# Performance work log

Hardware: AMD Instinct MI355X
Metric: run time of the kernel (lower is better)

## Reference

```python
import jax, jax.numpy as jnp
import numpy as np

EPS = 1e-5

def conv(x, w, b=None, groups=1):
    kh, kw = w.shape[2], w.shape[3]
    y = jax.lax.conv_general_dilated(
        x, w, (1, 1), ((kh // 2, kh // 2), (kw // 2, kw // 2)),
        dimension_numbers=('NCHW', 'OIHW', 'NCHW'), feature_group_count=groups)
    if b is not None:
        y = y + b[None, :, None, None]
    return y

def layernorm_c(x, g, b):
    # LayerNorm over channel dim (module permutes to NHWC, norms last dim, permutes back)
    mu = jnp.mean(x, axis=1, keepdims=True)
    var = jnp.mean(jnp.square(x - mu), axis=1, keepdims=True)
    return (x - mu) * jax.lax.rsqrt(var + EPS) * g[None, :, None, None] + b[None, :, None, None]

def _bilinear(img, py, px):
    # img: (N,C,H,W); py,px: (N,H,W) float sampling coords; zero outside bounds
    H, W = img.shape[2], img.shape[3]
    y0 = jnp.floor(py); x0 = jnp.floor(px)
    wy1 = py - y0; wy0 = 1.0 - wy1
    wx1 = px - x0; wx0 = 1.0 - wx1

    def gather(yc, xc):
        valid = (yc >= 0) & (yc <= H - 1) & (xc >= 0) & (xc <= W - 1)
        yi = jnp.clip(yc, 0, H - 1).astype(jnp.int32)
        xi = jnp.clip(xc, 0, W - 1).astype(jnp.int32)
        v = jax.vmap(lambda im, yy, xx: im[:, yy, xx])(img, yi, xi)  # (N,C,H,W)
        return v * valid[:, None].astype(img.dtype)

    return (gather(y0, x0) * (wy0 * wx0)[:, None]
            + gather(y0, x0 + 1) * (wy0 * wx1)[:, None]
            + gather(y0 + 1, x0) * (wy1 * wx0)[:, None]
            + gather(y0 + 1, x0 + 1) * (wy1 * wx1)[:, None])

def deform_conv2d(x, offset, weight, mask):
    # torchvision-style modulated deformable conv, 3x3, pad=1, stride=1
    N, C, H, W = x.shape
    by, bx = jnp.meshgrid(jnp.arange(H, dtype=x.dtype), jnp.arange(W, dtype=x.dtype), indexing='ij')
    out = jnp.zeros((N, weight.shape[0], H, W), dtype=x.dtype)
    for i in range(3):
        for j in range(3):
            k = i * 3 + j
            py = by[None] + (i - 1) + offset[:, 2 * k]      # (N,H,W)
            px = bx[None] + (j - 1) + offset[:, 2 * k + 1]
            samp = _bilinear(x, py, px) * mask[:, k][:, None]  # (N,C,H,W)
            out = out + jnp.einsum('nchw,oc->nohw', samp, weight[:, :, i, j])
    return out

def _forward(input_flow, input_event,
             ln_flow_g, ln_flow_b, ln_event_g, ln_event_b,
             ff_w1, ff_b1, ff_w2, ff_b2,
             fo_w1, fo_b1, fo_w2, fo_b2,
             fm_w1, fm_b1, fm_w2, fm_b2,
             dc_weight,
             sf_w1, sf_b1, sf_w2, sf_b2, sf_w3, sf_b3, sf_w4, sf_b4,
             fl_w1, fl_b1, fl_w2, fl_b2):
    N, C, H, W = input_flow.shape
    flow_norm = layernorm_c(input_flow, ln_flow_g, ln_flow_b)
    event_norm = layernorm_c(input_event, ln_event_g, ln_event_b)
    x = conv(jax.nn.relu(conv(flow_norm, ff_w1, ff_b1)), ff_w2, ff_b2, groups=C)
    offset = conv(jax.nn.relu(conv(event_norm, fo_w1, fo_b1)), fo_w2, fo_b2)
    mask = jax.nn.sigmoid(conv(jax.nn.relu(conv(event_norm, fm_w1, fm_b1)), fm_w2, fm_b2))
    dc = deform_conv2d(x, offset, dc_weight, mask)
    x_fft = jnp.fft.rfft2(x)            # (N,C,H,W//2+1) complex
    dc_fft = jnp.fft.rfft2(dc)
    fft_cate = jnp.concatenate([dc_fft.real, dc_fft.imag], axis=1)  # (N,2C,H,Wf)
    h = conv(fft_cate, sf_w1, sf_b1)
    h = conv(h, sf_w2, sf_b2, groups=2 * C)
    h = jax.nn.relu(conv(h, sf_w3, sf_b3))
    sp_mask = jax.nn.sigmoid(conv(h, sf_w4, sf_b4))  # (N,C,H,Wf) real
    x_irfft = jnp.fft.irfft2(x_fft * sp_mask, s=(H, W))
    g = conv(x_irfft, fl_w1, fl_b1, groups=C)
    a, b = jnp.split(g, 2, axis=1)
    g = a * jax.nn.gelu(b, approximate=False)
    return conv(g, fl_w2, fl_b2) + input_flow

def setup_inputs() -> dict:
    key = jax.random.key(0)
    N, C, H, W = 8, 32, 256, 256
    ks = iter(jax.random.split(key, 64))
    rn = lambda shp, s=0.05: jax.random.normal(next(ks), shp, dtype=jnp.float32) * s
    d = {
        'input_flow': jax.random.normal(next(ks), (N, C, H, W), dtype=jnp.float32),
        'input_event': jax.random.normal(next(ks), (N, C, H, W), dtype=jnp.float32),
        'ln_flow_g': 1.0 + rn((C,), 0.1), 'ln_flow_b': rn((C,), 0.1),
        'ln_event_g': 1.0 + rn((C,), 0.1), 'ln_event_b': rn((C,), 0.1),
        'ff_w1': rn((C, C, 1, 1)), 'ff_b1': rn((C,)),
        'ff_w2': rn((C, 1, 3, 3)), 'ff_b2': rn((C,)),
        'fo_w1': rn((C, C, 1, 1)), 'fo_b1': rn((C,)),
        'fo_w2': rn((18, C, 3, 3)), 'fo_b2': rn((18,)),
        'fm_w1': rn((C, C, 1, 1)), 'fm_b1': rn((C,)),
        'fm_w2': rn((9, C, 3, 3)), 'fm_b2': rn((9,)),
        'dc_weight': rn((C, C, 3, 3)),
        'sf_w1': rn((2 * C, 2 * C, 1, 1)), 'sf_b1': rn((2 * C,)),
        'sf_w2': rn((2 * C, 1, 3, 3)), 'sf_b2': rn((2 * C,)),
        'sf_w3': rn((2 * C, 2 * C, 1, 1)), 'sf_b3': rn((2 * C,)),
        'sf_w4': rn((C, 2 * C, 1, 1)), 'sf_b4': rn((C,)),
        'fl_w1': rn((C, 1, 3, 3)), 'fl_b1': rn((C,)),
        'fl_w2': rn((C, C // 2, 1, 1)), 'fl_b2': rn((C,)),
    }
    return d

def reference(input_flow, input_event,
              ln_flow_g, ln_flow_b, ln_event_g, ln_event_b,
              ff_w1, ff_b1, ff_w2, ff_b2,
              fo_w1, fo_b1, fo_w2, fo_b2,
              fm_w1, fm_b1, fm_w2, fm_b2,
              dc_weight,
              sf_w1, sf_b1, sf_w2, sf_b2, sf_w3, sf_b3, sf_w4, sf_b4,
              fl_w1, fl_b1, fl_w2, fl_b2):
    return _forward(input_flow, input_event,
                    ln_flow_g, ln_flow_b, ln_event_g, ln_event_b,
                    ff_w1, ff_b1, ff_w2, ff_b2,
                    fo_w1, fo_b1, fo_w2, fo_b2,
                    fm_w1, fm_b1, fm_w2, fm_b2,
                    dc_weight,
                    sf_w1, sf_b1, sf_w2, sf_b2, sf_w3, sf_b3, sf_w4, sf_b4,
                    fl_w1, fl_b1, fl_w2, fl_b2)
```

## Files before the change

kernel.cpp:

```cpp
#include <hip/hip_runtime.h>
#include <cmath>

constexpr int kN = 8;
constexpr int kC = 32;
constexpr int kH = 256;
constexpr int kW = 256;
constexpr int kHW = kH * kW;
constexpr int kWF = 129;
constexpr int kHWF = kH * kWF;
constexpr float kPI = 3.14159265358979323846f;

__device__ __forceinline__ float sigmoidf_(float x) { return 1.f / (1.f + expf(-x)); }

__device__ __forceinline__ int xcd_swizzle(int bid, int nblk)
{
    int chunk = nblk >> 3;
    return (bid & 7) * chunk + (bid >> 3);
}

template <bool TWO>
__global__ __launch_bounds__(256) void lnmv_kernel(
    const float* __restrict__ in,
    const float* __restrict__ lng, const float* __restrict__ lnb,
    const float* __restrict__ w1, const float* __restrict__ b1, float* __restrict__ out1,
    const float* __restrict__ w2, const float* __restrict__ b2, float* __restrict__ out2)
{
    __shared__ __align__(16) float wl1[1024];
    __shared__ __align__(16) float wl2[TWO ? 1024 : 4];
    __shared__ float bl1[32], bl2[32], gl[32], bbl[32];
    int tid = threadIdx.x;
    for (int e = tid; e < 1024; e += 256) {
        wl1[e] = w1[e];
        if (TWO) wl2[e] = w2[e];
    }
    if (tid < 32) {
        bl1[tid] = b1[tid]; gl[tid] = lng[tid]; bbl[tid] = lnb[tid];
        if (TWO) bl2[tid] = b2[tid];
    }
    __syncthreads();

    int p = blockIdx.x * 256 + tid;
    int n = p >> 16;
    int rem = p & 65535;
    const float* base = in + (size_t)n * kC * kHW + rem;

    float v[32];
    float mu = 0.f;
#pragma unroll
    for (int c = 0; c < 32; ++c) { v[c] = base[(size_t)c * kHW]; mu += v[c]; }
    mu *= 0.03125f;
    float var = 0.f;
#pragma unroll
    for (int c = 0; c < 32; ++c) { float d = v[c] - mu; var += d * d; }
    var *= 0.03125f;
    float rs = rsqrtf(var + 1e-5f);
#pragma unroll
    for (int c = 0; c < 32; ++c) v[c] = (v[c] - mu) * rs * gl[c] + bbl[c];

    {
        float* o = out1 + (size_t)n * kC * kHW + rem;
#pragma unroll
        for (int oc = 0; oc < 32; ++oc) {
            const float4* wr = reinterpret_cast<const float4*>(wl1 + oc * 32);
            float acc = bl1[oc];
#pragma unroll
            for (int q = 0; q < 8; ++q) {
                float4 wv = wr[q];
                acc += wv.x * v[4*q] + wv.y * v[4*q+1] + wv.z * v[4*q+2] + wv.w * v[4*q+3];
            }
            o[(size_t)oc * kHW] = fmaxf(acc, 0.f);
        }
    }
    if (TWO) {
        float* o = out2 + (size_t)n * kC * kHW + rem;
#pragma unroll
        for (int oc = 0; oc < 32; ++oc) {
            const float4* wr = reinterpret_cast<const float4*>(wl2 + oc * 32);
            float acc = bl2[oc];
#pragma unroll
            for (int q = 0; q < 8; ++q) {
                float4 wv = wr[q];
                acc += wv.x * v[4*q] + wv.y * v[4*q+1] + wv.z * v[4*q+2] + wv.w * v[4*q+3];
            }
            o[(size_t)oc * kHW] = fmaxf(acc, 0.f);
        }
    }
}

__global__ __launch_bounds__(256) void dw3x3_kernel(
    const float* __restrict__ in, const float* __restrict__ w,
    const float* __restrict__ bias, float* __restrict__ out,
    int CH, int Hd, int Wd, int total)
{
    int sw = xcd_swizzle(blockIdx.x, gridDim.x);
    int idx = sw * 256 + threadIdx.x;
    if (idx >= total) return;
    int wx = idx % Wd;
    int rest = idx / Wd;
    int hy = rest % Hd;
    int pl = rest / Hd;
    int ch = pl % CH;

    const float* ip = in + (size_t)pl * Hd * Wd;
    const float* wp = w + ch * 9;
    float acc = bias[ch];
#pragma unroll
    for (int dy = -1; dy <= 1; ++dy) {
        int yy = hy + dy;
        if (yy < 0 || yy >= Hd) continue;
        const float* rp = ip + (size_t)yy * Wd;
#pragma unroll
        for (int dx = -1; dx <= 1; ++dx) {
            int xx = wx + dx;
            if (xx < 0 || xx >= Wd) continue;
            acc += rp[xx] * wp[(dy + 1) * 3 + (dx + 1)];
        }
    }
    out[idx] = acc;
}

template <int COUT, int COUTP, int ACT>
__global__ __launch_bounds__(256) void conv3x3_kernel(
    const float* __restrict__ in, const float* __restrict__ wg,
    const float* __restrict__ bias, float* __restrict__ out)
{
    __shared__ __align__(16) float wl[288 * COUTP];
    __shared__ float bl[COUT];
    int tid = threadIdx.x;
    for (int e = tid; e < 288 * COUTP; e += 256) {
        int oc = e % COUTP;
        int t = e / COUTP;
        wl[e] = (oc < COUT) ? wg[(oc * 32 + (t / 9)) * 9 + (t % 9)] : 0.f;
    }
    if (tid < COUT) bl[tid] = bias[tid];
    __syncthreads();

    int sw = xcd_swizzle(blockIdx.x, gridDim.x);
    int row = sw * 4 + (tid >> 6);
    int lane = tid & 63;
    int n = row >> 8;
    int h = row & 255;

    float acc[4][COUTP];
#pragma unroll
    for (int px = 0; px < 4; ++px)
#pragma unroll
        for (int oc = 0; oc < COUTP; ++oc) acc[px][oc] = (oc < COUT) ? bl[oc] : 0.f;

    const float* ib = in + (size_t)n * 32 * kHW;
    for (int ic = 0; ic < 32; ++ic) {
        const float* ipl = ib + (size_t)ic * kHW;
#pragma unroll
        for (int ky = 0; ky < 3; ++ky) {
            int yy = h + ky - 1;
            if (yy < 0 || yy > 255) continue;
            const float* rp = ipl + (size_t)yy * 256;
#pragma unroll
            for (int kx = 0; kx < 3; ++kx) {
                float val[4];
#pragma unroll
                for (int px = 0; px < 4; ++px) {
                    int xx = lane + px * 64 + kx - 1;
                    val[px] = (xx >= 0 && xx < 256) ? rp[xx] : 0.f;
                }
                const float4* wr = reinterpret_cast<const float4*>(wl + (ic * 9 + ky * 3 + kx) * COUTP);
#pragma unroll
                for (int q = 0; q < COUTP / 4; ++q) {
                    float4 wv = wr[q];
#pragma unroll
                    for (int px = 0; px < 4; ++px) {
                        acc[px][4*q+0] += val[px] * wv.x;
                        acc[px][4*q+1] += val[px] * wv.y;
                        acc[px][4*q+2] += val[px] * wv.z;
                        acc[px][4*q+3] += val[px] * wv.w;
                    }
                }
            }
        }
    }

    float* ob = out + (size_t)n * COUT * kHW + (size_t)h * 256;
#pragma unroll
    for (int oc = 0; oc < COUT; ++oc) {
#pragma unroll
        for (int px = 0; px < 4; ++px) {
            float r = acc[px][oc];
            if (ACT == 2) r = sigmoidf_(r);
            ob[(size_t)oc * kHW + lane + px * 64] = r;
        }
    }
}

__global__ __launch_bounds__(256) void deform_kernel(
    const float* __restrict__ x, const float* __restrict__ off,
    const float* __restrict__ msk, const float* __restrict__ wt,
    float* __restrict__ out)
{
    __shared__ __align__(16) float wl[9 * 32 * 32];
    int tid = threadIdx.x;
    for (int e = tid; e < 9216; e += 256) {
        int o = e & 31;
        int t = e >> 5;
        int c = t & 31;
        int k = t >> 5;
        wl[e] = wt[((size_t)(o * 32 + c)) * 9 + k];
    }
    __syncthreads();

    int sw = xcd_swizzle(blockIdx.x, gridDim.x);
    int halfid = tid >> 7;
    int l = tid & 127;
    int row = sw * 2 + halfid;
    int n = row >> 8;
    int h = row & 255;
    int pixbase = h * 256 + l;

    const float* offb = off + (size_t)n * 18 * kHW + pixbase;
    const float* mskb = msk + (size_t)n * 9 * kHW + pixbase;
    const float* xb = x + (size_t)n * 32 * kHW;

    float acc[2][32];
#pragma unroll
    for (int px = 0; px < 2; ++px)
#pragma unroll
        for (int oc = 0; oc < 32; ++oc) acc[px][oc] = 0.f;

    for (int k = 0; k < 9; ++k) {
        int ki = k / 3 - 1, kj = k % 3 - 1;
        int i00[2], i01[2], i10[2], i11[2];
        float w00[2], w01[2], w10[2], w11[2];
#pragma unroll
        for (int px = 0; px < 2; ++px) {
            int wx = l + px * 128;
            float oy = offb[(size_t)(2 * k) * kHW + px * 128];
            float ox = offb[(size_t)(2 * k + 1) * kHW + px * 128];
            float m = mskb[(size_t)k * kHW + px * 128];
            float py = (float)(h + ki) + oy;
            float pxx = (float)(wx + kj) + ox;
            float y0f = floorf(py), x0f = floorf(pxx);
            float fy = py - y0f, fx = pxx - x0f;
            float vy0 = (y0f >= 0.f && y0f <= 255.f) ? 1.f : 0.f;
            float vy1 = (y0f >= -1.f && y0f <= 254.f) ? 1.f : 0.f;
            float vx0 = (x0f >= 0.f && x0f <= 255.f) ? 1.f : 0.f;
            float vx1 = (x0f >= -1.f && x0f <= 254.f) ? 1.f : 0.f;
            int y0 = min(max((int)y0f, 0), 255);
            int y1 = min(max((int)y0f + 1, 0), 255);
            int x0 = min(max((int)x0f, 0), 255);
            int x1 = min(max((int)x0f + 1, 0), 255);
            i00[px] = y0 * 256 + x0; i01[px] = y0 * 256 + x1;
            i10[px] = y1 * 256 + x0; i11[px] = y1 * 256 + x1;
            w00[px] = (1.f - fy) * (1.f - fx) * m * vy0 * vx0;
            w01[px] = (1.f - fy) * fx * m * vy0 * vx1;
            w10[px] = fy * (1.f - fx) * m * vy1 * vx0;
            w11[px] = fy * fx * m * vy1 * vx1;
        }
#pragma unroll 2
        for (int c = 0; c < 32; ++c) {
            const float* xp = xb + (size_t)c * kHW;
            float s[2];
#pragma unroll
            for (int px = 0; px < 2; ++px) {
                s[px] = w00[px] * xp[i00[px]] + w01[px] * xp[i01[px]] +
                        w10[px] * xp[i10[px]] + w11[px] * xp[i11[px]];
            }
            const float4* wr = reinterpret_cast<const float4*>(wl + (size_t)(k * 32 + c) * 32);
#pragma unroll
            for (int q = 0; q < 8; ++q) {
                float4 wv = wr[q];
#pragma unroll
                for (int px = 0; px < 2; ++px) {
                    acc[px][4*q+0] += s[px] * wv.x;
                    acc[px][4*q+1] += s[px] * wv.y;
                    acc[px][4*q+2] += s[px] * wv.z;
                    acc[px][4*q+3] += s[px] * wv.w;
                }
            }
        }
    }

    float* ob = out + (size_t)n * 32 * kHW + pixbase;
#pragma unroll
    for (int oc = 0; oc < 32; ++oc)
#pragma unroll
        for (int px = 0; px < 2; ++px)
            ob[(size_t)oc * kHW + px * 128] = acc[px][oc];
}

__device__ __forceinline__ void fft256_stages(float2* A, float2* Bb, const float2* tw,
                                              int lane, float sgn)
{
    float2* src = A;
    float2* dst = Bb;
#pragma unroll
    for (int s = 0; s < 4; ++s) {
        int m = 1 << (2 * s);
        int r = lane & (m - 1);
        int mc = lane - r;
        __syncthreads();
        float2 x0 = src[lane];
        float2 x1 = src[lane + 128];
        float2 x2 = src[lane + 64];
        float2 x3 = src[lane + 192];
        float2 wa = tw[mc];
        float2 wb = tw[mc + 64];
        float2 wc = tw[2 * mc];
        float way = wa.y * sgn, wby = wb.y * sgn, wcy = wc.y * sgn;
        float e1x = x0.x + x1.x, e1y = x0.y + x1.y;
        float d1x = x0.x - x1.x, d1y = x0.y - x1.y;
        float o1x = wa.x * d1x - way * d1y, o1y = wa.x * d1y + way * d1x;
        float e2x = x2.x + x3.x, e2y = x2.y + x3.y;
        float d2x = x2.x - x3.x, d2y = x2.y - x3.y;
        float o2x = wb.x * d2x - wby * d2y, o2y = wb.x * d2y + wby * d2x;
        int base = r + 4 * mc;
        float2 y0; y0.x = e1x + e2x; y0.y = e1y + e2y;
        float ex = e1x - e2x, ey = e1y - e2y;
        float2 y2; y2.x = wc.x * ex - wcy * ey; y2.y = wc.x * ey + wcy * ex;
        float2 y1; y1.x = o1x + o2x; y1.y = o1y + o2y;
        float ox = o1x - o2x, oy = o1y - o2y;
        float2 y3; y3.x = wc.x * ox - wcy * oy; y3.y = wc.x * oy + wcy * ox;
        dst[base] = y0;
        dst[base + m] = y1;
        dst[base + 2 * m] = y2;
        dst[base + 3 * m] = y3;
        float2* t = src; src = dst; dst = t;
    }
    __syncthreads();
}

__device__ __forceinline__ void fft256_stages16(float2* A, float2* Bb, const float2* tw,
                                                int t, int c, float sgn)
{
    float2* src = A;
    float2* dst = Bb;
#pragma unroll
    for (int s = 0; s < 4; ++s) {
        int m = 1 << (2 * s);
        __syncthreads();
#pragma unroll
        for (int b = 0; b < 4; ++b) {
            int q = t + (b << 4);
            int r = q & (m - 1);
            int mc = q - r;
            float2 x0 = src[q * 17 + c];
            float2 x1 = src[(q + 128) * 17 + c];
            float2 x2 = src[(q + 64) * 17 + c];
            float2 x3 = src[(q + 192) * 17 + c];
            float2 wa = tw[mc];
            float2 wb = tw[mc + 64];
            float2 wc = tw[2 * mc];
            float way = wa.y * sgn, wby = wb.y * sgn, wcy = wc.y * sgn;
            float e1x = x0.x + x1.x, e1y = x0.y + x1.y;
            float d1x = x0.x - x1.x, d1y = x0.y - x1.y;
            float o1x = wa.x * d1x - way * d1y, o1y = wa.x * d1y + way * d1x;
            float e2x = x2.x + x3.x, e2y = x2.y + x3.y;
            float d2x = x2.x - x3.x, d2y = x2.y - x3.y;
            float o2x = wb.x * d2x - wby * d2y, o2y = wb.x * d2y + wby * d2x;
            int base = r + 4 * mc;
            float2 y0; y0.x = e1x + e2x; y0.y = e1y + e2y;
            float ex = e1x - e2x, ey = e1y - e2y;
            float2 y2; y2.x = wc.x * ex - wcy * ey; y2.y = wc.x * ey + wcy * ex;
            float2 y1; y1.x = o1x + o2x; y1.y = o1y + o2y;
            float ox = o1x - o2x, oy = o1y - o2y;
            float2 y3; y3.x = wc.x * ox - wcy * oy; y3.y = wc.x * oy + wcy * ox;
            dst[base * 17 + c] = y0;
            dst[(base + m) * 17 + c] = y1;
            dst[(base + 2 * m) * 17 + c] = y2;
            dst[(base + 3 * m) * 17 + c] = y3;
        }
        float2* tp = src; src = dst; dst = tp;
    }
    __syncthreads();
}

__device__ __forceinline__ void make_tw(float2* tw, int tid)
{
    if (tid < 128) {
        float ang = -kPI * (float)tid / 128.f;
        float2 w; w.x = cosf(ang); w.y = sinf(ang);
        tw[tid] = w;
    }
}

__global__ __launch_bounds__(256) void fft_rows_r2c(const float* __restrict__ in,
                                                    float2* __restrict__ out)
{
    __shared__ float2 A[4][256];
    __shared__ float2 Bb[4][256];
    __shared__ float2 tw[128];
    int tid = threadIdx.x;
    int sub = tid >> 6, lane = tid & 63;
    make_tw(tw, tid);
    size_t row = (size_t)blockIdx.x * 4 + sub;
    const float* rp = in + row * 256;
#pragma unroll
    for (int r = 0; r < 4; ++r) {
        int i = lane + 64 * r;
        float2 a; a.x = rp[i]; a.y = 0.f;
        A[sub][i] = a;
    }
    fft256_stages(A[sub], Bb[sub], tw, lane, 1.f);
    float2* op = out + row * kWF;
    op[lane] = A[sub][lane];
    op[lane + 64] = A[sub][lane + 64];
    if (lane == 0) op[128] = A[sub][128];
}

__global__ __launch_bounds__(256) void fft_cols16(float2* __restrict__ buf)
{
    __shared__ float2 A[256 * 17];
    __shared__ float2 Bb[256 * 17];
    __shared__ float2 tw[128];
    int tid = threadIdx.x;
    make_tw(tw, tid);
    int b = xcd_swizzle(blockIdx.x, gridDim.x);
    int p = b / 9;
    int grp = b % 9;
    int col0 = grp * 16;
    int ncols = (col0 + 16 <= kWF) ? 16 : (kWF - col0);
    float2* base = buf + (size_t)p * kHWF + col0;
    for (int e = tid; e < 4096; e += 256) {
        int pp = e >> 4, cc = e & 15;
        if (cc < ncols) A[pp * 17 + cc] = base[(size_t)pp * kWF + cc];
    }
    int c = tid & 15, t = tid >> 4;
    fft256_stages16(A, Bb, tw, t, c, 1.f);
    for (int e = tid; e < 4096; e += 256) {
        int pp = e >> 4, cc = e & 15;
        if (cc < ncols) base[(size_t)pp * kWF + cc] = A[pp * 17 + cc];
    }
}

__global__ __launch_bounds__(256) void ifft_cols_mask16(const float2* __restrict__ xf,
                                                        const float* __restrict__ spm,
                                                        float2* __restrict__ out)
{
    __shared__ float2 A[256 * 17];
    __shared__ float2 Bb[256 * 17];
    __shared__ float2 tw[128];
    int tid = threadIdx.x;
    make_tw(tw, tid);
    int b = xcd_swizzle(blockIdx.x, gridDim.x);
    int p = b / 9;
    int grp = b % 9;
    int col0 = grp * 16;
    int ncols = (col0 + 16 <= kWF) ? 16 : (kWF - col0);
    const float2* xb = xf + (size_t)p * kHWF + col0;
    const float* mb = spm + (size_t)p * kHWF + col0;
    for (int e = tid; e < 4096; e += 256) {
        int pp = e >> 4, cc = e & 15;
        if (cc < ncols) {
            float2 a = xb[(size_t)pp * kWF + cc];
            float m = mb[(size_t)pp * kWF + cc];
            a.x *= m; a.y *= m;
            A[pp * 17 + cc] = a;
        }
    }
    int c = tid & 15, t = tid >> 4;
    fft256_stages16(A, Bb, tw, t, c, -1.f);
    float2* ob = out + (size_t)p * kHWF + col0;
    for (int e = tid; e < 4096; e += 256) {
        int pp = e >> 4, cc = e & 15;
        if (cc < ncols) ob[(size_t)pp * kWF + cc] = A[pp * 17 + cc];
    }
}

__global__ __launch_bounds__(256) void ifft_rows_c2r(const float2* __restrict__ in,
                                                     float* __restrict__ out)
{
    __shared__ float2 A[4][256];
    __shared__ float2 Bb[4][256];
    __shared__ float2 tw[128];
    int tid = threadIdx.x;
    int sub = tid >> 6, lane = tid & 63;
    make_tw(tw, tid);
    size_t row = (size_t)blockIdx.x * 4 + sub;
    const float2* ip = in + row * kWF;
#pragma unroll
    for (int r = 0; r < 4; ++r) {
        int k = lane + 64 * r;
        if (k <= 128) {
            A[sub][k] = ip[k];
        } else {
            float2 c = ip[256 - k];
            c.y = -c.y;
            A[sub][k] = c;
        }
    }
    fft256_stages(A[sub], Bb[sub], tw, lane, -1.f);
    float* op = out + row * 256;
#pragma unroll
    for (int r = 0; r < 4; ++r) {
        int k = lane + 64 * r;
        op[k] = A[sub][k].x * (1.f / 65536.f);
    }
}

template <int CIN, int COUT, int ACT, bool CPLX>
__global__ __launch_bounds__(256) void conv1x1_kernel(
    const void* __restrict__ inv, const float* __restrict__ wg,
    const float* __restrict__ bias, float* __restrict__ out)
{
    constexpr int PL = kHWF;
    __shared__ __align__(16) float wl[COUT * CIN];
    __shared__ float bl[COUT];
    int tid = threadIdx.x;
    for (int e = tid; e < COUT * CIN; e += 256) wl[e] = wg[e];
    if (tid < COUT) bl[tid] = bias[tid];
    __syncthreads();

    int p0 = blockIdx.x * 256 + tid;
    int n0 = p0 / PL, r0 = p0 % PL;

    float v0[CIN];
    if (CPLX) {
        const float2* in2 = (const float2*)inv;
#pragma unroll
        for (int c = 0; c < 32; ++c) {
            float2 a = in2[(size_t)(n0 * 32 + c) * PL + r0];
            v0[c] = a.x; v0[32 + c] = a.y;
        }
    } else {
        const float* inf_ = (const float*)inv;
#pragma unroll
        for (int c = 0; c < CIN; ++c) {
            v0[c] = inf_[(size_t)(n0 * CIN + c) * PL + r0];
        }
    }

#pragma unroll
    for (int oc = 0; oc < COUT; ++oc) {
        const float4* wr = reinterpret_cast<const float4*>(wl + oc * CIN);
        float a0 = bl[oc];
#pragma unroll
        for (int q = 0; q < CIN / 4; ++q) {
            float4 wv = wr[q];
            a0 += wv.x * v0[4*q] + wv.y * v0[4*q+1] + wv.z * v0[4*q+2] + wv.w * v0[4*q+3];
        }
        if (ACT == 1) a0 = fmaxf(a0, 0.f);
        if (ACT == 2) a0 = sigmoidf_(a0);
        out[(size_t)(n0 * COUT + oc) * PL + r0] = a0;
    }
}

__global__ __launch_bounds__(256) void conv1x1_chain_kernel(
    const float* __restrict__ in, const float* __restrict__ w3,
    const float* __restrict__ b3, const float* __restrict__ w4,
    const float* __restrict__ b4, float* __restrict__ out)
{
    constexpr int PL = kHWF;
    __shared__ __align__(16) float wl3[64 * 64];
    __shared__ __align__(16) float wl4[32 * 64];
    __shared__ float bl3[64], bl4[32];
    int tid = threadIdx.x;
    for (int e = tid; e < 4096; e += 256) wl3[e] = w3[e];
    for (int e = tid; e < 2048; e += 256) wl4[e] = w4[e];
    if (tid < 64) bl3[tid] = b3[tid];
    if (tid < 32) bl4[tid] = b4[tid];
    __syncthreads();

    int p0 = blockIdx.x * 256 + tid;
    int n0 = p0 / PL, r0 = p0 % PL;

    float v0[64];
#pragma unroll
    for (int c = 0; c < 64; ++c) v0[c] = in[(size_t)(n0 * 64 + c) * PL + r0];

    float t0[64];
#pragma unroll
    for (int oc = 0; oc < 64; ++oc) {
        const float4* wr = reinterpret_cast<const float4*>(wl3 + oc * 64);
        float a0 = bl3[oc];
#pragma unroll
        for (int q = 0; q < 16; ++q) {
            float4 wv = wr[q];
            a0 += wv.x * v0[4*q] + wv.y * v0[4*q+1] + wv.z * v0[4*q+2] + wv.w * v0[4*q+3];
        }
        t0[oc] = fmaxf(a0, 0.f);
    }

#pragma unroll
    for (int oc = 0; oc < 32; ++oc) {
        const float4* wr = reinterpret_cast<const float4*>(wl4 + oc * 64);
        float a0 = bl4[oc];
#pragma unroll
        for (int q = 0; q < 16; ++q) {
            float4 wv = wr[q];
            a0 += wv.x * t0[4*q] + wv.y * t0[4*q+1] + wv.z * t0[4*q+2] + wv.w * t0[4*q+3];
        }
        out[(size_t)(n0 * 32 + oc) * PL + r0] = sigmoidf_(a0);
    }
}

__global__ __launch_bounds__(256) void final_kernel(
    const float* __restrict__ g, const float* __restrict__ flow,
    const float* __restrict__ wg, const float* __restrict__ bias,
    float* __restrict__ out)
{
    __shared__ __align__(16) float wl[32 * 16];
    __shared__ float bl[32];
    int tid = threadIdx.x;
    for (int e = tid; e < 512; e += 256) wl[e] = wg[e];
    if (tid < 32) bl[tid] = bias[tid];
    __syncthreads();

    int p = blockIdx.x * 256 + tid;
    int n = p >> 16;
    int rem = p & 65535;
    const float* gb = g + (size_t)n * 32 * kHW + rem;

    float v[16];
#pragma unroll
    for (int c = 0; c < 16; ++c) {
        float a = gb[(size_t)c * kHW];
        float b = gb[(size_t)(16 + c) * kHW];
        float ge = 0.5f * b * (1.f + erff(b * 0.70710678118654752f));
        v[c] = a * ge;
    }

    const float* fb = flow + (size_t)n * 32 * kHW + rem;
    float* ob = out + (size_t)n * 32 * kHW + rem;
#pragma unroll
    for (int oc = 0; oc < 32; ++oc) {
        const float4* wr = reinterpret_cast<const float4*>(wl + oc * 16);
        float acc = bl[oc];
#pragma unroll
        for (int q = 0; q < 4; ++q) {
            float4 wv = wr[q];
            acc += wv.x * v[4*q] + wv.y * v[4*q+1] + wv.z * v[4*q+2] + wv.w * v[4*q+3];
        }
        ob[(size_t)oc * kHW] = acc + fb[(size_t)oc * kHW];
    }
}

extern "C" void kernel_launch(void* const* d_in, const int* in_sizes, int n_in,
                              void* d_out, int out_size, void* d_ws, size_t ws_size,
                              hipStream_t stream)
{
    (void)in_sizes; (void)n_in; (void)out_size; (void)ws_size;

    const float* input_flow  = (const float*)d_in[0];
    const float* input_event = (const float*)d_in[1];
    const float* ln_flow_g   = (const float*)d_in[2];
    const float* ln_flow_b   = (const float*)d_in[3];
    const float* ln_event_g  = (const float*)d_in[4];
    const float* ln_event_b  = (const float*)d_in[5];
    const float* ff_w1 = (const float*)d_in[6];
    const float* ff_b1 = (const float*)d_in[7];
    const float* ff_w2 = (const float*)d_in[8];
    const float* ff_b2 = (const float*)d_in[9];
    const float* fo_w1 = (const float*)d_in[10];
    const float* fo_b1 = (const float*)d_in[11];
    const float* fo_w2 = (const float*)d_in[12];
    const float* fo_b2 = (const float*)d_in[13];
    const float* fm_w1 = (const float*)d_in[14];
    const float* fm_b1 = (const float*)d_in[15];
    const float* fm_w2 = (const float*)d_in[16];
    const float* fm_b2 = (const float*)d_in[17];
    const float* dc_weight = (const float*)d_in[18];
    const float* sf_w1 = (const float*)d_in[19];
    const float* sf_b1 = (const float*)d_in[20];
    const float* sf_w2 = (const float*)d_in[21];
    const float* sf_b2 = (const float*)d_in[22];
    const float* sf_w3 = (const float*)d_in[23];
    const float* sf_b3 = (const float*)d_in[24];
    const float* sf_w4 = (const float*)d_in[25];
    const float* sf_b4 = (const float*)d_in[26];
    const float* fl_w1 = (const float*)d_in[27];
    const float* fl_b1 = (const float*)d_in[28];
    const float* fl_w2 = (const float*)d_in[29];
    const float* fl_b2 = (const float*)d_in[30];
    float* out = (float*)d_out;

    const size_t S = (size_t)16908288;
    float* A = (float*)d_ws;
    float* B = A + S;
    float* Cs = B + S;
    float* X = out;

    lnmv_kernel<false><<<2048, 256, 0, stream>>>(input_flow, ln_flow_g, ln_flow_b,
                                                 ff_w1, ff_b1, A,
                                                 nullptr, nullptr, nullptr);
    lnmv_kernel<true><<<2048, 256, 0, stream>>>(input_event, ln_event_g, ln_event_b,
                                                fo_w1, fo_b1, B,
                                                fm_w1, fm_b1, Cs);
    dw3x3_kernel<<<65536, 256, 0, stream>>>(A, ff_w2, ff_b2, X, 32, 256, 256, 16777216);
    conv3x3_kernel<18, 20, 0><<<512, 256, 0, stream>>>(B, fo_w2, fo_b2, A);
    conv3x3_kernel<9, 12, 2><<<512, 256, 0, stream>>>(Cs, fm_w2, fm_b2, B);
    deform_kernel<<<1024, 256, 0, stream>>>(X, A, B, dc_weight, Cs);
    fft_rows_r2c<<<16384, 256, 0, stream>>>(X, (float2*)A);
    fft_cols16<<<2304, 256, 0, stream>>>((float2*)A);
    fft_rows_r2c<<<16384, 256, 0, stream>>>(Cs, (float2*)B);
    fft_cols16<<<2304, 256, 0, stream>>>((float2*)B);
    conv1x1_kernel<64, 64, 0, true><<<1032, 256, 0, stream>>>((const void*)B, sf_w1, sf_b1, Cs);
    dw3x3_kernel<<<66048, 256, 0, stream>>>(Cs, sf_w2, sf_b2, B, 64, 256, 129, 16908288);
    conv1x1_chain_kernel<<<1032, 256, 0, stream>>>(B, sf_w3, sf_b3, sf_w4, sf_b4, Cs);
    ifft_cols_mask16<<<2304, 256, 0, stream>>>((const float2*)A, Cs, (float2*)B);
    ifft_rows_c2r<<<16384, 256, 0, stream>>>((const float2*)B, Cs);
    dw3x3_kernel<<<65536, 256, 0, stream>>>(Cs, fl_w1, fl_b1, A, 32, 256, 256, 16777216);
    final_kernel<<<2048, 256, 0, stream>>>(A, input_flow, fl_w2, fl_b2, out);
}
```

Before: 1.447 ms.

## Split output channels across blocks in offset conv and deformable conv kernels

The 18-output-channel offset conv now splits its output channels into two halves of 9 handled by separate blocks, doubling the grid. The deformable conv kernel is restructured so each block covers 16 output channels and 4 rows at 4 pixels per thread, instead of 32 channels over 2 rows. The goal is more blocks and lower per-thread register pressure, which should raise occupancy. The cost is redundant input loads and bilinear gathers, since every sample is now computed twice, once per channel half.

```diff
diff --git a/kernel.cpp b/kernel.cpp
--- a/kernel.cpp
+++ b/kernel.cpp
@@ -119,24 +119,26 @@
     out[idx] = acc;
 }
 
-template <int COUT, int COUTP, int ACT>
+template <int COUTTOT, int COUTH, int COUTP, int ACT, int NSPL>
 __global__ __launch_bounds__(256) void conv3x3_kernel(
     const float* __restrict__ in, const float* __restrict__ wg,
     const float* __restrict__ bias, float* __restrict__ out)
 {
     __shared__ __align__(16) float wl[288 * COUTP];
-    __shared__ float bl[COUT];
-    int tid = threadIdx.x;
+    __shared__ float bl[COUTH];
+    int tid = threadIdx.x;
+    int sw = xcd_swizzle(blockIdx.x, gridDim.x);
+    int rowblk = sw / NSPL;
+    int ocbase = (sw % NSPL) * COUTH;
     for (int e = tid; e < 288 * COUTP; e += 256) {
         int oc = e % COUTP;
         int t = e / COUTP;
-        wl[e] = (oc < COUT) ? wg[(oc * 32 + (t / 9)) * 9 + (t % 9)] : 0.f;
-    }
-    if (tid < COUT) bl[tid] = bias[tid];
+        wl[e] = (oc < COUTH) ? wg[((ocbase + oc) * 32 + (t / 9)) * 9 + (t % 9)] : 0.f;
+    }
+    if (tid < COUTH) bl[tid] = bias[ocbase + tid];
     __syncthreads();
 
-    int sw = xcd_swizzle(blockIdx.x, gridDim.x);
-    int row = sw * 4 + (tid >> 6);
+    int row = rowblk * 4 + (tid >> 6);
     int lane = tid & 63;
     int n = row >> 8;
     int h = row & 255;
@@ -145,7 +147,7 @@
 #pragma unroll
     for (int px = 0; px < 4; ++px)
 #pragma unroll
-        for (int oc = 0; oc < COUTP; ++oc) acc[px][oc] = (oc < COUT) ? bl[oc] : 0.f;
+        for (int oc = 0; oc < COUTP; ++oc) acc[px][oc] = (oc < COUTH) ? bl[oc] : 0.f;
 
     const float* ib = in + (size_t)n * 32 * kHW;
     for (int ic = 0; ic < 32; ++ic) {
@@ -179,9 +181,9 @@
         }
     }
 
-    float* ob = out + (size_t)n * COUT * kHW + (size_t)h * 256;
-#pragma unroll
-    for (int oc = 0; oc < COUT; ++oc) {
+    float* ob = out + (size_t)n * COUTTOT * kHW + (size_t)ocbase * kHW + (size_t)h * 256;
+#pragma unroll
+    for (int oc = 0; oc < COUTH; ++oc) {
 #pragma unroll
         for (int px = 0; px < 4; ++px) {
             float r = acc[px][oc];
@@ -196,45 +198,46 @@
     const float* __restrict__ msk, const float* __restrict__ wt,
     float* __restrict__ out)
 {
-    __shared__ __align__(16) float wl[9 * 32 * 32];
-    int tid = threadIdx.x;
-    for (int e = tid; e < 9216; e += 256) {
-        int o = e & 31;
-        int t = e >> 5;
+    __shared__ __align__(16) float wl[9 * 32 * 16];
+    int tid = threadIdx.x;
+    int sw = xcd_swizzle(blockIdx.x, gridDim.x);
+    int rowblk = sw >> 1;
+    int ocbase = (sw & 1) * 16;
+    for (int e = tid; e < 4608; e += 256) {
+        int o = e & 15;
+        int t = e >> 4;
         int c = t & 31;
         int k = t >> 5;
-        wl[e] = wt[((size_t)(o * 32 + c)) * 9 + k];
+        wl[e] = wt[((size_t)((ocbase + o) * 32 + c)) * 9 + k];
     }
     __syncthreads();
 
-    int sw = xcd_swizzle(blockIdx.x, gridDim.x);
-    int halfid = tid >> 7;
-    int l = tid & 127;
-    int row = sw * 2 + halfid;
+    int row = rowblk * 4 + (tid >> 6);
+    int lane = tid & 63;
     int n = row >> 8;
     int h = row & 255;
-    int pixbase = h * 256 + l;
+    int pixbase = h * 256 + lane;
 
     const float* offb = off + (size_t)n * 18 * kHW + pixbase;
     const float* mskb = msk + (size_t)n * 9 * kHW + pixbase;
     const float* xb = x + (size_t)n * 32 * kHW;
 
-    float acc[2][32];
-#pragma unroll
-    for (int px = 0; px < 2; ++px)
-#pragma unroll
-        for (int oc = 0; oc < 32; ++oc) acc[px][oc] = 0.f;
+    float acc[4][16];
+#pragma unroll
+    for (int px = 0; px < 4; ++px)
+#pragma unroll
+        for (int oc = 0; oc < 16; ++oc) acc[px][oc] = 0.f;
 
     for (int k = 0; k < 9; ++k) {
         int ki = k / 3 - 1, kj = k % 3 - 1;
-        int i00[2], i01[2], i10[2], i11[2];
-        float w00[2], w01[2], w10[2], w11[2];
-#pragma unroll
-        for (int px = 0; px < 2; ++px) {
-            int wx = l + px * 128;
-            float oy = offb[(size_t)(2 * k) * kHW + px * 128];
-            float ox = offb[(size_t)(2 * k + 1) * kHW + px * 128];
-            float m = mskb[(size_t)k * kHW + px * 128];
+        int i00[4], i01[4], i10[4], i11[4];
+        float w00[4], w01[4], w10[4], w11[4];
+#pragma unroll
+        for (int px = 0; px < 4; ++px) {
+            int wx = lane + px * 64;
+            float oy = offb[(size_t)(2 * k) * kHW + px * 64];
+            float ox = offb[(size_t)(2 * k + 1) * kHW + px * 64];
+            float m = mskb[(size_t)k * kHW + px * 64];
             float py = (float)(h + ki) + oy;
             float pxx = (float)(wx + kj) + ox;
             float y0f = floorf(py), x0f = floorf(pxx);
@@ -254,21 +257,20 @@
             w10[px] = fy * (1.f - fx) * m * vy1 * vx0;
             w11[px] = fy * fx * m * vy1 * vx1;
         }
-#pragma unroll 2
         for (int c = 0; c < 32; ++c) {
             const float* xp = xb + (size_t)c * kHW;
-            float s[2];
-#pragma unroll
-            for (int px = 0; px < 2; ++px) {
+            float s[4];
+#pragma unroll
+            for (int px = 0; px < 4; ++px) {
                 s[px] = w00[px] * xp[i00[px]] + w01[px] * xp[i01[px]] +
                         w10[px] * xp[i10[px]] + w11[px] * xp[i11[px]];
             }
-            const float4* wr = reinterpret_cast<const float4*>(wl + (size_t)(k * 32 + c) * 32);
-#pragma unroll
-            for (int q = 0; q < 8; ++q) {
+            const float4* wr = reinterpret_cast<const float4*>(wl + (size_t)(k * 32 + c) * 16);
+#pragma unroll
+            for (int q = 0; q < 4; ++q) {
                 float4 wv = wr[q];
 #pragma unroll
-                for (int px = 0; px < 2; ++px) {
+                for (int px = 0; px < 4; ++px) {
                     acc[px][4*q+0] += s[px] * wv.x;
                     acc[px][4*q+1] += s[px] * wv.y;
                     acc[px][4*q+2] += s[px] * wv.z;
@@ -278,12 +280,12 @@
         }
     }
 
-    float* ob = out + (size_t)n * 32 * kHW + pixbase;
-#pragma unroll
-    for (int oc = 0; oc < 32; ++oc)
-#pragma unroll
-        for (int px = 0; px < 2; ++px)
-            ob[(size_t)oc * kHW + px * 128] = acc[px][oc];
+    float* ob = out + (size_t)n * 32 * kHW + (size_t)ocbase * kHW + pixbase;
+#pragma unroll
+    for (int oc = 0; oc < 16; ++oc)
+#pragma unroll
+        for (int px = 0; px < 4; ++px)
+            ob[(size_t)oc * kHW + px * 64] = acc[px][oc];
 }
 
 __device__ __forceinline__ void fft256_stages(float2* A, float2* Bb, const float2* tw,
@@ -684,8 +686,8 @@
                                                 fo_w1, fo_b1, B,
                                                 fm_w1, fm_b1, Cs);
     dw3x3_kernel<<<65536, 256, 0, stream>>>(A, ff_w2, ff_b2, X, 32, 256, 256, 16777216);
-    conv3x3_kernel<18, 20, 0><<<512, 256, 0, stream>>>(B, fo_w2, fo_b2, A);
-    conv3x3_kernel<9, 12, 2><<<512, 256, 0, stream>>>(Cs, fm_w2, fm_b2, B);
+    conv3x3_kernel<18, 9, 12, 0, 2><<<1024, 256, 0, stream>>>(B, fo_w2, fo_b2, A);
+    conv3x3_kernel<9, 9, 12, 2, 1><<<512, 256, 0, stream>>>(Cs, fm_w2, fm_b2, B);
     deform_kernel<<<1024, 256, 0, stream>>>(X, A, B, dc_weight, Cs);
     fft_rows_r2c<<<16384, 256, 0, stream>>>(X, (float2*)A);
     fft_cols16<<<2304, 256, 0, stream>>>((float2*)A);
```

New measurement: 1.734 ms. +19.9%, slower.
